# Performance work log

Hardware: AMD Instinct MI355X
Metric: run time of the kernel (lower is better)

The kernel has to match this reference:

```python
import jax, jax.numpy as jnp
import numpy as np

H = 256            # hidden_dim
E = H // 2         # uniform_dim = 128
NH = 4             # num_heads
DH = E // NH       # head_dim = 32
OUT = 256          # output_dim
B = 65536
LN_EPS = 1e-5


def _lin(k, din, dout):
    kw, kb = jax.random.split(k)
    bound = 1.0 / np.sqrt(din)
    W = jax.random.uniform(kw, (din, dout), jnp.float32, -bound, bound)
    b = jax.random.uniform(kb, (dout,), jnp.float32, -bound, bound)
    return W, b


def setup_inputs() -> dict:
    key = jax.random.key(0)
    ks = jax.random.split(key, 20)
    x = jax.random.normal(ks[0], (B, 29), jnp.float32)
    # component encoders (Linear + ReLU)
    Wv, bv = _lin(ks[1], 3, H // 4)
    Wm, bm = _lin(ks[2], 5, H // 4)
    Wi, bi = _lin(ks[3], 2, H // 8)
    Wb, bb = _lin(ks[4], 3, H // 8)
    Wc, bc = _lin(ks[5], 6, H // 4)
    Wf, bf = _lin(ks[6], 10, H // 2)
    # projections to uniform_dim
    Pv, pv = _lin(ks[7], H // 4, E)
    Pm, pm = _lin(ks[8], H // 4, E)
    Pi, pi = _lin(ks[9], H // 8, E)
    Pb, pb = _lin(ks[10], H // 8, E)
    Pc, pc = _lin(ks[11], H // 4, E)
    Pf, pf = _lin(ks[12], H // 2, E)
    # multi-head attention (packed QKV in_proj + out_proj), stored as [in,out]
    Wqkv, bqkv = _lin(ks[13], E, 3 * E)
    Wo, bo = _lin(ks[14], E, E)
    # layernorm
    g = jnp.ones((E,), jnp.float32)
    beta = jnp.zeros((E,), jnp.float32)
    # pool projection
    Wp, bp = _lin(ks[15], E, OUT)
    return dict(x=x, Wv=Wv, bv=bv, Wm=Wm, bm=bm, Wi=Wi, bi=bi, Wb=Wb, bb=bb,
                Wc=Wc, bc=bc, Wf=Wf, bf=bf, Pv=Pv, pv=pv, Pm=Pm, pm=pm,
                Pi=Pi, pi=pi, Pb=Pb, pb=pb, Pc=Pc, pc=pc, Pf=Pf, pf=pf,
                Wqkv=Wqkv, bqkv=bqkv, Wo=Wo, bo=bo, g=g, beta=beta, Wp=Wp, bp=bp)


def _forward(x, Wv, bv, Wm, bm, Wi, bi, Wb, bb, Wc, bc, Wf, bf,
             Pv, pv, Pm, pm, Pi, pi, Pb, pb, Pc, pc, Pf, pf,
             Wqkv, bqkv, Wo, bo, g, beta, Wp, bp):
    enc = lambda v, W, b: jax.nn.relu(v @ W + b)
    # component encoders + projections -> 6 tokens of dim E
    t_v = enc(x[:, 0:3], Wv, bv) @ Pv + pv
    t_m = enc(x[:, 3:8], Wm, bm) @ Pm + pm
    t_i = enc(x[:, 8:10], Wi, bi) @ Pi + pi
    t_b = enc(x[:, 10:13], Wb, bb) @ Pb + pb
    t_c = enc(x[:, 13:19], Wc, bc) @ Pc + pc
    t_f = enc(x[:, 19:29], Wf, bf) @ Pf + pf
    tokens = jnp.stack([t_v, t_m, t_i, t_b, t_c, t_f], axis=1)  # [B,6,E]
    Bn = tokens.shape[0]
    # self-attention (torch MultiheadAttention, batch_first, eval mode)
    qkv = tokens @ Wqkv + bqkv                                   # [B,6,3E]
    q, k, v = jnp.split(qkv, 3, axis=-1)
    q = q.reshape(Bn, 6, NH, DH)
    k = k.reshape(Bn, 6, NH, DH)
    v = v.reshape(Bn, 6, NH, DH)
    scores = jnp.einsum('bqhd,bkhd->bhqk', q, k) / np.sqrt(DH)  # [B,H,6,6]
    attn = jax.nn.softmax(scores, axis=-1)
    ctx = jnp.einsum('bhqk,bkhd->bqhd', attn, v).reshape(Bn, 6, E)
    attn_out = ctx @ Wo + bo
    # residual + layernorm
    h = tokens + attn_out
    mu = jnp.mean(h, axis=-1, keepdims=True)
    var = jnp.mean(jnp.square(h - mu), axis=-1, keepdims=True)
    h = (h - mu) * jax.lax.rsqrt(var + LN_EPS) * g + beta
    # mean-pool over 6 tokens, project, relu
    pooled = jnp.mean(h, axis=1)                                 # [B,E]
    return jax.nn.relu(pooled @ Wp + bp)                         # [B,OUT]


def reference(x, Wv, bv, Wm, bm, Wi, bi, Wb, bb, Wc, bc, Wf, bf,
              Pv, pv, Pm, pm, Pi, pi, Pb, pb, Pc, pc, Pf, pf,
              Wqkv, bqkv, Wo, bo, g, beta, Wp, bp):
    return _forward(x, Wv, bv, Wm, bm, Wi, bi, Wb, bb, Wc, bc, Wf, bf,
                    Pv, pv, Pm, pm, Pi, pi, Pb, pb, Pc, pc, Pf, pf,
                    Wqkv, bqkv, Wo, bo, g, beta, Wp, bp)
```

## Files before the change

### kernel.cpp

```cpp
#include <hip/hip_runtime.h>
#include <math.h>

typedef float f32x4 __attribute__((ext_vector_type(4)));
typedef short short8 __attribute__((ext_vector_type(8)));
typedef unsigned short u16;

#define LN_EPS 1e-5f

__device__ __forceinline__ u16 f2bf(float f) {
    unsigned int x = __float_as_uint(f);
    return (u16)((x + 0x7fffu + ((x >> 16) & 1u)) >> 16);
}
__device__ __forceinline__ float bf2f(u16 u) {
    return __uint_as_float(((unsigned int)u) << 16);
}

#define OFF_QKV 0
#define OFF_WO  49152
#define OFF_WP  65536
#define OFF_PV  98304
#define OFF_PM  106496
#define OFF_PI  114688
#define OFF_PB  118784
#define OFF_PC  122880
#define OFF_PF  131072
#define WS_ELEMS 147456

__global__ __launch_bounds__(512) void convert_weights(
    const float* __restrict__ Wqkv, const float* __restrict__ Wo, const float* __restrict__ Wp,
    const float* __restrict__ Pv, const float* __restrict__ Pm, const float* __restrict__ Pi,
    const float* __restrict__ Pb, const float* __restrict__ Pc, const float* __restrict__ Pf,
    u16* __restrict__ ws)
{
    int gid = blockIdx.x * 512 + threadIdx.x;
    if (gid >= WS_ELEMS) return;
    const float* src; int N, Ksteps, local;
    if (gid < OFF_WO)      { src = Wqkv; N = 384; Ksteps = 4; local = gid; }
    else if (gid < OFF_WP) { src = Wo;   N = 128; Ksteps = 4; local = gid - OFF_WO; }
    else if (gid < OFF_PV) { src = Wp;   N = 256; Ksteps = 4; local = gid - OFF_WP; }
    else if (gid < OFF_PM) { src = Pv;   N = 128; Ksteps = 2; local = gid - OFF_PV; }
    else if (gid < OFF_PI) { src = Pm;   N = 128; Ksteps = 2; local = gid - OFF_PM; }
    else if (gid < OFF_PB) { src = Pi;   N = 128; Ksteps = 1; local = gid - OFF_PI; }
    else if (gid < OFF_PC) { src = Pb;   N = 128; Ksteps = 1; local = gid - OFF_PB; }
    else if (gid < OFF_PF) { src = Pc;   N = 128; Ksteps = 2; local = gid - OFF_PC; }
    else                   { src = Pf;   N = 128; Ksteps = 4; local = gid - OFF_PF; }
    int j  = local & 7;
    int l  = (local >> 3) & 63;
    int r2 = local >> 9;
    int kk = r2 % Ksteps;
    int nt = r2 / Ksteps;
    int srow = kk * 32 + (l >> 4) * 8 + j;
    int scol = nt * 16 + (l & 15);
    ws[gid] = f2bf(src[srow * N + scol]);
}

__global__ __launch_bounds__(512, 4) void asmlp_mfma(
    const float* __restrict__ x,
    const float* __restrict__ Wv, const float* __restrict__ bv,
    const float* __restrict__ Wm, const float* __restrict__ bm,
    const float* __restrict__ Wi, const float* __restrict__ bi,
    const float* __restrict__ Wb, const float* __restrict__ bb,
    const float* __restrict__ Wc, const float* __restrict__ bc,
    const float* __restrict__ Wf, const float* __restrict__ bf_,
    const float* __restrict__ pv, const float* __restrict__ pm,
    const float* __restrict__ pi_, const float* __restrict__ pb_,
    const float* __restrict__ pc_, const float* __restrict__ pf_,
    const float* __restrict__ bqkv, const float* __restrict__ bo,
    const float* __restrict__ gg, const float* __restrict__ beta,
    const float* __restrict__ bp,
    const u16* __restrict__ ws,
    float* __restrict__ out)
{
    const int blk  = blockIdx.x;
    const int t    = threadIdx.x;
    const int lane = t & 63;
    const int wv   = t >> 6;
    const int col  = lane & 15;
    const int lg   = lane >> 4;

    __shared__ u16 sm[31872];
    u16*   s_tok  = sm;
    u16*   s_qkv  = sm + 6144;
    u16*   s_ctx  = sm + 24576;
    u16*   s_att  = sm + 30720;
    float* s_x    = (float*)(sm + 24576);
    u16*   s_h    = sm + 25088;
    u16*   s_pool = sm + 30720;
    float* s_out  = (float*)(sm + 6144);

    if (t < 232) s_x[t] = x[(size_t)blk * 232 + t];
    __syncthreads();

    for (int i = 0; i < 6; ++i) {
        int u = t + i * 512;
        int row = u / 384;
        int jj = u - row * 384;
        const float* W; const float* bias; int din, xo, j, dout;
        if (jj < 64)       { W = Wv; bias = bv;  din = 3;  xo = 0;  j = jj;       dout = 64; }
        else if (jj < 128) { W = Wm; bias = bm;  din = 5;  xo = 3;  j = jj - 64;  dout = 64; }
        else if (jj < 160) { W = Wi; bias = bi;  din = 2;  xo = 8;  j = jj - 128; dout = 32; }
        else if (jj < 192) { W = Wb; bias = bb;  din = 3;  xo = 10; j = jj - 160; dout = 32; }
        else if (jj < 256) { W = Wc; bias = bc;  din = 6;  xo = 13; j = jj - 192; dout = 64; }
        else               { W = Wf; bias = bf_; din = 10; xo = 19; j = jj - 256; dout = 128; }
        float acc = bias[j];
        for (int i2 = 0; i2 < din; ++i2) acc += s_x[row * 29 + xo + i2] * W[i2 * dout + j];
        acc = fmaxf(acc, 0.f);
        s_h[((row * 48 + ((jj >> 3) ^ row)) << 3) + (jj & 7)] = f2bf(acc);
    }
    __syncthreads();

    for (int q = 0; q < 6; ++q) {
        int unit = wv * 6 + q;
        int c = unit >> 3, n = unit & 7;
        const float* bias; int ks, hg, wso;
        switch (c) {
            case 0:  bias = pv;  ks = 2; hg = 0;  wso = OFF_PV; break;
            case 1:  bias = pm;  ks = 2; hg = 8;  wso = OFF_PM; break;
            case 2:  bias = pi_; ks = 1; hg = 16; wso = OFF_PI; break;
            case 3:  bias = pb_; ks = 1; hg = 20; wso = OFF_PB; break;
            case 4:  bias = pc_; ks = 2; hg = 24; wso = OFF_PC; break;
            default: bias = pf_; ks = 4; hg = 32; wso = OFF_PF; break;
        }
        float bcol = bias[n * 16 + col];
        f32x4 acc = {bcol, bcol, bcol, bcol};
        int arow = col & 7;
        for (int kk = 0; kk < ks; ++kk) {
            int g = hg + kk * 4 + lg;
            short8 a = *(const short8*)&s_h[(arow * 48 + (g ^ arow)) << 3];
            short8 b = *(const short8*)&ws[wso + (((n * ks + kk) * 64 + lane) << 3)];
            acc = __builtin_amdgcn_mfma_f32_16x16x32_bf16(a, b, acc, 0, 0, 0);
        }
        if (lg < 2) {
            #pragma unroll
            for (int r = 0; r < 4; ++r) {
                int row = lg * 4 + r;
                int tok = c * 8 + row;
                int cn  = n * 16 + col;
                s_tok[((tok * 16 + ((cn >> 3) ^ (tok & 15))) << 3) + (cn & 7)] = f2bf(acc[r]);
            }
        }
    }
    __syncthreads();

    {
        short8 Bf[3][4];
        float  bb_[3];
        #pragma unroll
        for (int ni = 0; ni < 3; ++ni) {
            int n = wv * 3 + ni;
            bb_[ni] = bqkv[n * 16 + col];
            #pragma unroll
            for (int kk = 0; kk < 4; ++kk)
                Bf[ni][kk] = *(const short8*)&ws[OFF_QKV + (((n * 4 + kk) * 64 + lane) << 3)];
        }
        for (int mt = 0; mt < 3; ++mt) {
            int arow = mt * 16 + col;
            short8 A[4];
            #pragma unroll
            for (int kk = 0; kk < 4; ++kk) {
                int g = kk * 4 + lg;
                A[kk] = *(const short8*)&s_tok[(arow * 16 + (g ^ (arow & 15))) << 3];
            }
            #pragma unroll
            for (int ni = 0; ni < 3; ++ni) {
                f32x4 acc = {bb_[ni], bb_[ni], bb_[ni], bb_[ni]};
                #pragma unroll
                for (int kk = 0; kk < 4; ++kk)
                    acc = __builtin_amdgcn_mfma_f32_16x16x32_bf16(A[kk], Bf[ni][kk], acc, 0, 0, 0);
                int cn = (wv * 3 + ni) * 16 + col;
                #pragma unroll
                for (int r = 0; r < 4; ++r) {
                    int row = mt * 16 + lg * 4 + r;
                    s_qkv[((row * 48 + ((cn >> 3) ^ (row & 15))) << 3) + (cn & 7)] = f2bf(acc[r]);
                }
            }
        }
    }
    __syncthreads();

    if (t < 192) {
        int row = t / 24;
        int rem = t - row * 24;
        int h   = rem / 6;
        int qi  = rem - h * 6;
        int tq  = qi * 8 + row;
        float qf[32];
        #pragma unroll
        for (int gi = 0; gi < 4; ++gi) {
            int g = h * 4 + gi;
            short8 v = *(const short8*)&s_qkv[(tq * 48 + (g ^ (tq & 15))) << 3];
            #pragma unroll
            for (int j = 0; j < 8; ++j) qf[gi * 8 + j] = bf2f((u16)v[j]);
        }
        float sc[6];
        #pragma unroll
        for (int ki = 0; ki < 6; ++ki) {
            int tk = ki * 8 + row;
            float d = 0.f;
            #pragma unroll
            for (int gi = 0; gi < 4; ++gi) {
                int g = 16 + h * 4 + gi;
                short8 v = *(const short8*)&s_qkv[(tk * 48 + (g ^ (tk & 15))) << 3];
                #pragma unroll
                for (int j = 0; j < 8; ++j) d += qf[gi * 8 + j] * bf2f((u16)v[j]);
            }
            sc[ki] = d * 0.17677669529663687f;
        }
        float mx = sc[0];
        #pragma unroll
        for (int ki = 1; ki < 6; ++ki) mx = fmaxf(mx, sc[ki]);
        float e[6], s = 0.f;
        #pragma unroll
        for (int ki = 0; ki < 6; ++ki) { e[ki] = __expf(sc[ki] - mx); s += e[ki]; }
        float inv = 1.f / s;
        #pragma unroll
        for (int ki = 0; ki < 6; ++ki)
            s_att[((row * 4 + h) * 6 + qi) * 6 + ki] = f2bf(e[ki] * inv);
    }
    __syncthreads();

    for (int u = t; u < 768; u += 512) {
        int m = u >> 4, gch = u & 15;
        int row = m & 7, qi = m >> 3, h = gch >> 2;
        float accs[8] = {0, 0, 0, 0, 0, 0, 0, 0};
        #pragma unroll
        for (int ki = 0; ki < 6; ++ki) {
            float p = bf2f(s_att[((row * 4 + h) * 6 + qi) * 6 + ki]);
            int tv = ki * 8 + row;
            int g  = 32 + gch;
            short8 v = *(const short8*)&s_qkv[(tv * 48 + (g ^ (tv & 15))) << 3];
            #pragma unroll
            for (int j = 0; j < 8; ++j) accs[j] += p * bf2f((u16)v[j]);
        }
        short8 o;
        #pragma unroll
        for (int j = 0; j < 8; ++j) o[j] = (short)f2bf(accs[j]);
        *(short8*)&s_ctx[(m * 16 + (gch ^ (m & 15))) << 3] = o;
    }
    __syncthreads();

    if (wv < 3) {
        int mt = wv;
        int arow = mt * 16 + col;
        short8 A[4];
        #pragma unroll
        for (int kk = 0; kk < 4; ++kk) {
            int g = kk * 4 + lg;
            A[kk] = *(const short8*)&s_ctx[(arow * 16 + (g ^ (arow & 15))) << 3];
        }
        f32x4 acc[8];
        #pragma unroll
        for (int n = 0; n < 8; ++n) {
            float b = bo[n * 16 + col];
            acc[n] = (f32x4){b, b, b, b};
            #pragma unroll
            for (int kk = 0; kk < 4; ++kk) {
                short8 Bf = *(const short8*)&ws[OFF_WO + (((n * 4 + kk) * 64 + lane) << 3)];
                acc[n] = __builtin_amdgcn_mfma_f32_16x16x32_bf16(A[kk], Bf, acc[n], 0, 0, 0);
            }
        }
        #pragma unroll
        for (int n = 0; n < 8; ++n) {
            int cn = n * 16 + col;
            #pragma unroll
            for (int r = 0; r < 4; ++r) {
                int row = mt * 16 + lg * 4 + r;
                acc[n][r] += bf2f(s_tok[((row * 16 + ((cn >> 3) ^ (row & 15))) << 3) + (cn & 7)]);
            }
        }
        float mu_[4], rs_[4];
        #pragma unroll
        for (int r = 0; r < 4; ++r) {
            float s1 = 0.f, s2 = 0.f;
            #pragma unroll
            for (int n = 0; n < 8; ++n) { float v = acc[n][r]; s1 += v; s2 += v * v; }
            #pragma unroll
            for (int off = 1; off <= 8; off <<= 1) {
                s1 += __shfl_xor(s1, off, 64);
                s2 += __shfl_xor(s2, off, 64);
            }
            float mu  = s1 * (1.f / 128.f);
            float var = s2 * (1.f / 128.f) - mu * mu;
            mu_[r] = mu;
            rs_[r] = rsqrtf(var + LN_EPS);
        }
        #pragma unroll
        for (int n = 0; n < 8; ++n) {
            int cn = n * 16 + col;
            float gw = gg[cn], bw = beta[cn];
            #pragma unroll
            for (int r = 0; r < 4; ++r) {
                int row = mt * 16 + lg * 4 + r;
                float val = (acc[n][r] - mu_[r]) * rs_[r] * gw + bw;
                s_tok[((row * 16 + ((cn >> 3) ^ (row & 15))) << 3) + (cn & 7)] = f2bf(val);
            }
        }
    }
    __syncthreads();

    if (t < 128) {
        int row = t >> 4, gch = t & 15;
        float fa[8] = {0, 0, 0, 0, 0, 0, 0, 0};
        #pragma unroll
        for (int c = 0; c < 6; ++c) {
            int tok = c * 8 + row;
            short8 v = *(const short8*)&s_tok[(tok * 16 + (gch ^ (tok & 15))) << 3];
            #pragma unroll
            for (int j = 0; j < 8; ++j) fa[j] += bf2f((u16)v[j]);
        }
        short8 o;
        #pragma unroll
        for (int j = 0; j < 8; ++j) o[j] = (short)f2bf(fa[j] * (1.f / 6.f));
        *(short8*)&s_pool[(row * 16 + (gch ^ row)) << 3] = o;
    }
    __syncthreads();

    {
        int arow = col & 7;
        short8 A[4];
        #pragma unroll
        for (int kk = 0; kk < 4; ++kk) {
            int g = kk * 4 + lg;
            A[kk] = *(const short8*)&s_pool[(arow * 16 + (g ^ arow)) << 3];
        }
        #pragma unroll
        for (int ni = 0; ni < 2; ++ni) {
            int n = wv * 2 + ni;
            float b = bp[n * 16 + col];
            f32x4 acc = {b, b, b, b};
            #pragma unroll
            for (int kk = 0; kk < 4; ++kk) {
                short8 Bf = *(const short8*)&ws[OFF_WP + (((n * 4 + kk) * 64 + lane) << 3)];
                acc = __builtin_amdgcn_mfma_f32_16x16x32_bf16(A[kk], Bf, acc, 0, 0, 0);
            }
            if (lg < 2) {
                #pragma unroll
                for (int r = 0; r < 4; ++r) {
                    int row = lg * 4 + r;
                    s_out[row * 260 + n * 16 + col] = fmaxf(acc[r], 0.f);
                }
            }
        }
    }
    __syncthreads();

    if (t < 256) {
        int row = t >> 5, c8 = (t & 31) * 8;
        f32x4 v0 = *(const f32x4*)&s_out[row * 260 + c8];
        f32x4 v1 = *(const f32x4*)&s_out[row * 260 + c8 + 4];
        float* dst = out + ((size_t)blk * 8 + row) * 256 + c8;
        *(f32x4*)dst = v0;
        *(f32x4*)(dst + 4) = v1;
    }
}

extern "C" void kernel_launch(void* const* d_in, const int* in_sizes, int n_in,
                              void* d_out, int out_size, void* d_ws, size_t ws_size,
                              hipStream_t stream) {
    const float* x    = (const float*)d_in[0];
    const float* Wv   = (const float*)d_in[1];
    const float* bv   = (const float*)d_in[2];
    const float* Wm   = (const float*)d_in[3];
    const float* bm   = (const float*)d_in[4];
    const float* Wi   = (const float*)d_in[5];
    const float* bi   = (const float*)d_in[6];
    const float* Wb   = (const float*)d_in[7];
    const float* bb   = (const float*)d_in[8];
    const float* Wc   = (const float*)d_in[9];
    const float* bc   = (const float*)d_in[10];
    const float* Wf   = (const float*)d_in[11];
    const float* bf_  = (const float*)d_in[12];
    const float* Pv   = (const float*)d_in[13];
    const float* pv   = (const float*)d_in[14];
    const float* Pm   = (const float*)d_in[15];
    const float* pm   = (const float*)d_in[16];
    const float* Pi   = (const float*)d_in[17];
    const float* pii  = (const float*)d_in[18];
    const float* Pb   = (const float*)d_in[19];
    const float* pb   = (const float*)d_in[20];
    const float* Pc   = (const float*)d_in[21];
    const float* pc   = (const float*)d_in[22];
    const float* Pf   = (const float*)d_in[23];
    const float* pf   = (const float*)d_in[24];
    const float* Wqkv = (const float*)d_in[25];
    const float* bqkv = (const float*)d_in[26];
    const float* Wo   = (const float*)d_in[27];
    const float* bo   = (const float*)d_in[28];
    const float* gg   = (const float*)d_in[29];
    const float* beta = (const float*)d_in[30];
    const float* Wp   = (const float*)d_in[31];
    const float* bp   = (const float*)d_in[32];
    float* out = (float*)d_out;
    u16* ws = (u16*)d_ws;

    convert_weights<<<288, 512, 0, stream>>>(Wqkv, Wo, Wp, Pv, Pm, Pi, Pb, Pc, Pf, ws);

    const int Bn = in_sizes[0] / 29;
    asmlp_mfma<<<Bn / 8, 512, 0, stream>>>(
        x, Wv, bv, Wm, bm, Wi, bi, Wb, bb, Wc, bc, Wf, bf_,
        pv, pm, pii, pb, pc, pf,
        bqkv, bo, gg, beta, bp, ws, out);
}
```

Baseline: 338.1 us.

## Move encoder layers and attention score/context computation onto MFMA

The scalar component-encoder loop is replaced by a block-diagonal bf16 MFMA GEMM, with x split into hi/lo bf16 parts to keep precision. The weights and biases for it are pre-packed in the conversion kernel. Attention scores, softmax via lane shuffles, and the probability-times-V product now run as small MFMA tiles over transposed Q/K and V layouts instead of per-thread scalar dot products. The f32-to-bf16 rounding uses the packed hardware convert instruction. This cuts VALU work and the LDS footprint, at the cost of padding waste in the 6x6 attention tiles and more complex indexing.

```diff
diff --git a/kernel.cpp b/kernel.cpp
--- a/kernel.cpp
+++ b/kernel.cpp
@@ -7,12 +7,14 @@
 
 #define LN_EPS 1e-5f
 
-__device__ __forceinline__ u16 f2bf(float f) {
-    unsigned int x = __float_as_uint(f);
-    return (u16)((x + 0x7fffu + ((x >> 16) & 1u)) >> 16);
+__device__ __forceinline__ unsigned cvt_pk_bf16(float lo, float hi) {
+    unsigned r;
+    asm("v_cvt_pk_bf16_f32 %0, %1, %2" : "=v"(r) : "v"(lo), "v"(hi));
+    return r;
 }
+__device__ __forceinline__ u16 f2bf(float f) { return (u16)cvt_pk_bf16(f, f); }
 __device__ __forceinline__ float bf2f(u16 u) {
-    return __uint_as_float(((unsigned int)u) << 16);
+    return __uint_as_float(((unsigned)u) << 16);
 }
 
 #define OFF_QKV 0
@@ -24,44 +26,72 @@
 #define OFF_PB  118784
 #define OFF_PC  122880
 #define OFF_PF  131072
-#define WS_ELEMS 147456
+#define OFF_WENC 147456
+#define OFF_BENC 172032
+#define CW_TOTAL 172416
 
 __global__ __launch_bounds__(512) void convert_weights(
     const float* __restrict__ Wqkv, const float* __restrict__ Wo, const float* __restrict__ Wp,
     const float* __restrict__ Pv, const float* __restrict__ Pm, const float* __restrict__ Pi,
     const float* __restrict__ Pb, const float* __restrict__ Pc, const float* __restrict__ Pf,
+    const float* __restrict__ Wv, const float* __restrict__ Wm, const float* __restrict__ Wi,
+    const float* __restrict__ Wb, const float* __restrict__ Wc, const float* __restrict__ Wf,
+    const float* __restrict__ bv, const float* __restrict__ bm, const float* __restrict__ bi,
+    const float* __restrict__ bb, const float* __restrict__ bc, const float* __restrict__ bf_,
     u16* __restrict__ ws)
 {
     int gid = blockIdx.x * 512 + threadIdx.x;
-    if (gid >= WS_ELEMS) return;
-    const float* src; int N, Ksteps, local;
-    if (gid < OFF_WO)      { src = Wqkv; N = 384; Ksteps = 4; local = gid; }
-    else if (gid < OFF_WP) { src = Wo;   N = 128; Ksteps = 4; local = gid - OFF_WO; }
-    else if (gid < OFF_PV) { src = Wp;   N = 256; Ksteps = 4; local = gid - OFF_WP; }
-    else if (gid < OFF_PM) { src = Pv;   N = 128; Ksteps = 2; local = gid - OFF_PV; }
-    else if (gid < OFF_PI) { src = Pm;   N = 128; Ksteps = 2; local = gid - OFF_PM; }
-    else if (gid < OFF_PB) { src = Pi;   N = 128; Ksteps = 1; local = gid - OFF_PI; }
-    else if (gid < OFF_PC) { src = Pb;   N = 128; Ksteps = 1; local = gid - OFF_PB; }
-    else if (gid < OFF_PF) { src = Pc;   N = 128; Ksteps = 2; local = gid - OFF_PC; }
-    else                   { src = Pf;   N = 128; Ksteps = 4; local = gid - OFF_PF; }
-    int j  = local & 7;
-    int l  = (local >> 3) & 63;
-    int r2 = local >> 9;
-    int kk = r2 % Ksteps;
-    int nt = r2 / Ksteps;
-    int srow = kk * 32 + (l >> 4) * 8 + j;
-    int scol = nt * 16 + (l & 15);
-    ws[gid] = f2bf(src[srow * N + scol]);
+    if (gid < OFF_WENC) {
+        const float* src; int N, Ksteps, local;
+        if (gid < OFF_WO)      { src = Wqkv; N = 384; Ksteps = 4; local = gid; }
+        else if (gid < OFF_WP) { src = Wo;   N = 128; Ksteps = 4; local = gid - OFF_WO; }
+        else if (gid < OFF_PV) { src = Wp;   N = 256; Ksteps = 4; local = gid - OFF_WP; }
+        else if (gid < OFF_PM) { src = Pv;   N = 128; Ksteps = 2; local = gid - OFF_PV; }
+        else if (gid < OFF_PI) { src = Pm;   N = 128; Ksteps = 2; local = gid - OFF_PM; }
+        else if (gid < OFF_PB) { src = Pi;   N = 128; Ksteps = 1; local = gid - OFF_PI; }
+        else if (gid < OFF_PC) { src = Pb;   N = 128; Ksteps = 1; local = gid - OFF_PB; }
+        else if (gid < OFF_PF) { src = Pc;   N = 128; Ksteps = 2; local = gid - OFF_PC; }
+        else                   { src = Pf;   N = 128; Ksteps = 4; local = gid - OFF_PF; }
+        int j  = local & 7;
+        int l  = (local >> 3) & 63;
+        int r2 = local >> 9;
+        int kk = r2 % Ksteps;
+        int nt = r2 / Ksteps;
+        int srow = kk * 32 + (l >> 4) * 8 + j;
+        int scol = nt * 16 + (l & 15);
+        ws[gid] = f2bf(src[srow * N + scol]);
+    } else if (gid < OFF_BENC) {
+        int local = gid - OFF_WENC;
+        int j = local & 7, l = (local >> 3) & 63, r2 = local >> 9;
+        int kk = r2 & 1, nt = r2 >> 1;
+        int k = kk * 32 + (l >> 4) * 8 + j;
+        int r = k & 31;
+        int scol = nt * 16 + (l & 15);
+        const float* W; int cb, xo, din, dout;
+        if (scol < 64)       { W = Wv; cb = 0;   xo = 0;  din = 3;  dout = 64; }
+        else if (scol < 128) { W = Wm; cb = 64;  xo = 3;  din = 5;  dout = 64; }
+        else if (scol < 160) { W = Wi; cb = 128; xo = 8;  din = 2;  dout = 32; }
+        else if (scol < 192) { W = Wb; cb = 160; xo = 10; din = 3;  dout = 32; }
+        else if (scol < 256) { W = Wc; cb = 192; xo = 13; din = 6;  dout = 64; }
+        else                 { W = Wf; cb = 256; xo = 19; din = 10; dout = 128; }
+        int rr = r - xo;
+        float val = (r < 29 && rr >= 0 && rr < din) ? W[rr * dout + (scol - cb)] : 0.f;
+        ws[gid] = f2bf(val);
+    } else if (gid < CW_TOTAL) {
+        int j = gid - OFF_BENC;
+        const float* b; int off;
+        if (j < 64)       { b = bv;  off = 0; }
+        else if (j < 128) { b = bm;  off = 64; }
+        else if (j < 160) { b = bi;  off = 128; }
+        else if (j < 192) { b = bb;  off = 160; }
+        else if (j < 256) { b = bc;  off = 192; }
+        else              { b = bf_; off = 256; }
+        ((float*)(ws + OFF_BENC))[j] = b[j - off];
+    }
 }
 
 __global__ __launch_bounds__(512, 4) void asmlp_mfma(
     const float* __restrict__ x,
-    const float* __restrict__ Wv, const float* __restrict__ bv,
-    const float* __restrict__ Wm, const float* __restrict__ bm,
-    const float* __restrict__ Wi, const float* __restrict__ bi,
-    const float* __restrict__ Wb, const float* __restrict__ bb,
-    const float* __restrict__ Wc, const float* __restrict__ bc,
-    const float* __restrict__ Wf, const float* __restrict__ bf_,
     const float* __restrict__ pv, const float* __restrict__ pm,
     const float* __restrict__ pi_, const float* __restrict__ pb_,
     const float* __restrict__ pc_, const float* __restrict__ pf_,
@@ -78,37 +108,60 @@
     const int col  = lane & 15;
     const int lg   = lane >> 4;
 
-    __shared__ u16 sm[31872];
+    __shared__ __attribute__((aligned(16))) u16 sm[30720];
     u16*   s_tok  = sm;
-    u16*   s_qkv  = sm + 6144;
-    u16*   s_ctx  = sm + 24576;
-    u16*   s_att  = sm + 30720;
-    float* s_x    = (float*)(sm + 24576);
-    u16*   s_h    = sm + 25088;
-    u16*   s_pool = sm + 30720;
-    float* s_out  = (float*)(sm + 6144);
-
-    if (t < 232) s_x[t] = x[(size_t)blk * 232 + t];
-    __syncthreads();
-
-    for (int i = 0; i < 6; ++i) {
-        int u = t + i * 512;
-        int row = u / 384;
-        int jj = u - row * 384;
-        const float* W; const float* bias; int din, xo, j, dout;
-        if (jj < 64)       { W = Wv; bias = bv;  din = 3;  xo = 0;  j = jj;       dout = 64; }
-        else if (jj < 128) { W = Wm; bias = bm;  din = 5;  xo = 3;  j = jj - 64;  dout = 64; }
-        else if (jj < 160) { W = Wi; bias = bi;  din = 2;  xo = 8;  j = jj - 128; dout = 32; }
-        else if (jj < 192) { W = Wb; bias = bb;  din = 3;  xo = 10; j = jj - 160; dout = 32; }
-        else if (jj < 256) { W = Wc; bias = bc;  din = 6;  xo = 13; j = jj - 192; dout = 64; }
-        else               { W = Wf; bias = bf_; din = 10; xo = 19; j = jj - 256; dout = 128; }
-        float acc = bias[j];
-        for (int i2 = 0; i2 < din; ++i2) acc += s_x[row * 29 + xo + i2] * W[i2 * dout + j];
-        acc = fmaxf(acc, 0.f);
-        s_h[((row * 48 + ((jj >> 3) ^ row)) << 3) + (jj & 7)] = f2bf(acc);
-    }
-    __syncthreads();
-
+    u16*   s_qk   = sm + 6144;
+    u16*   s_vt   = sm + 18432;
+    u16*   s_ppad = sm + 26624;
+    u16*   s_xa   = sm + 18432;
+    u16*   s_h    = sm + 18944;
+    u16*   s_ctx  = sm + 6144;
+    float* s_out  = (float*)(sm + 12288);
+    u16*   s_pool = sm + 26624;
+
+    if (t < 232) {
+        int row = t / 29, cc = t - row * 29;
+        float f = x[(size_t)blk * 232 + t];
+        u16 hi = f2bf(f);
+        float lo = f - bf2f(hi);
+        s_xa[row * 64 + cc]      = hi;
+        s_xa[row * 64 + 32 + cc] = f2bf(lo);
+    }
+    if (t < 48) {
+        int row = t / 6, sl = t - (t / 6) * 6;
+        int k = (sl < 3) ? (29 + sl) : (58 + sl);
+        s_xa[row * 64 + k] = 0;
+    }
+    __syncthreads();
+
+    {
+        int arow = col & 7;
+        short8 A0 = *(const short8*)&s_xa[arow * 64 + lg * 8];
+        short8 A1 = *(const short8*)&s_xa[arow * 64 + 32 + lg * 8];
+        const float* benc = (const float*)(ws + OFF_BENC);
+        #pragma unroll
+        for (int q = 0; q < 3; ++q) {
+            int nt = wv * 3 + q;
+            float b = benc[nt * 16 + col];
+            f32x4 acc = {b, b, b, b};
+            short8 B0 = *(const short8*)&ws[OFF_WENC + (((nt * 2 + 0) * 64 + lane) << 3)];
+            short8 B1 = *(const short8*)&ws[OFF_WENC + (((nt * 2 + 1) * 64 + lane) << 3)];
+            acc = __builtin_amdgcn_mfma_f32_16x16x32_bf16(A0, B0, acc, 0, 0, 0);
+            acc = __builtin_amdgcn_mfma_f32_16x16x32_bf16(A1, B1, acc, 0, 0, 0);
+            if (lg < 2) {
+                #pragma unroll
+                for (int r = 0; r < 4; ++r) {
+                    int row = lg * 4 + r;
+                    int cn = nt * 16 + col;
+                    s_h[((row * 48 + ((cn >> 3) ^ row)) << 3) + (cn & 7)] =
+                        f2bf(fmaxf(acc[r], 0.f));
+                }
+            }
+        }
+    }
+    __syncthreads();
+
+    #pragma unroll
     for (int q = 0; q < 6; ++q) {
         int unit = wv * 6 + q;
         int c = unit >> 3, n = unit & 7;
@@ -153,9 +206,10 @@
             for (int kk = 0; kk < 4; ++kk)
                 Bf[ni][kk] = *(const short8*)&ws[OFF_QKV + (((n * 4 + kk) * 64 + lane) << 3)];
         }
+        { uint2 z; z.x = 0u; z.y = 0u; *(uint2*)&s_vt[t * 16 + 12] = z; }
         for (int mt = 0; mt < 3; ++mt) {
+            short8 A[4];
             int arow = mt * 16 + col;
-            short8 A[4];
             #pragma unroll
             for (int kk = 0; kk < 4; ++kk) {
                 int g = kk * 4 + lg;
@@ -167,75 +221,113 @@
                 #pragma unroll
                 for (int kk = 0; kk < 4; ++kk)
                     acc = __builtin_amdgcn_mfma_f32_16x16x32_bf16(A[kk], Bf[ni][kk], acc, 0, 0, 0);
-                int cn = (wv * 3 + ni) * 16 + col;
+                int cn = wv * 3 + ni;
+                int cg = cn * 16 + col;
+                if (cn < 16) {
+                    int q4 = ((cg >> 3) & 3) << 2;
+                    int tb = (mt * 16 + lg * 4) ^ q4;
+                    uint2 w;
+                    w.x = cvt_pk_bf16(acc[0], acc[1]);
+                    w.y = cvt_pk_bf16(acc[2], acc[3]);
+                    *(uint2*)&s_qk[cg * 48 + tb] = w;
+                } else {
+                    int d = cg - 256;
+                    int h = d >> 5, ch = (d >> 4) & 1, nn = d & 15;
+                    #pragma unroll
+                    for (int r = 0; r < 4; ++r) {
+                        int token = mt * 16 + lg * 4 + r;
+                        int c2 = token >> 3, rb = token & 7;
+                        int g2 = rb * 2 + (h >> 1);
+                        int kidx = (h & 1) * 6 + c2;
+                        s_vt[((g2 * 2 + ch) * 16 + nn) * 16 + kidx] = f2bf(acc[r]);
+                    }
+                }
+            }
+        }
+    }
+    __syncthreads();
+
+    {
+        const int rb = wv;
+        #pragma unroll
+        for (int i = 0; i < 2; ++i) {
+            const int hp = i;
+            int p  = (col >= 6 && col < 12) ? 1 : 0;
+            int qi = (col < 6) ? col : ((col < 12) ? col - 6 : 0);
+            int tt = qi * 8 + rb;
+            int h  = hp * 2 + p;
+            int tsw = tt ^ (lg << 2);
+            int abase = (h * 32 + lg * 8) * 48 + tsw;
+            int bbase = (128 + h * 32 + lg * 8) * 48 + tsw;
+            short8 Aq, Bk;
+            #pragma unroll
+            for (int j = 0; j < 8; ++j) {
+                Aq[j] = (short)s_qk[abase + j * 48];
+                Bk[j] = (short)s_qk[bbase + j * 48];
+            }
+            f32x4 sc = {0.f, 0.f, 0.f, 0.f};
+            sc = __builtin_amdgcn_mfma_f32_16x16x32_bf16(Aq, Bk, sc, 0, 0, 0);
+            u16* pp = s_ppad + (wv * 2 + i) * 256;
+            f32x4 pr4;
+            #pragma unroll
+            for (int r = 0; r < 4; ++r) {
+                int mr = lg * 4 + r;
+                int prr = (mr >= 6 && mr < 12) ? 1 : 0;
+                float v = sc[r] * 0.17677669529663687f;
+                bool inR = (col >= 6 * prr) && (col < 6 * prr + 6);
+                float mv = inR ? v : -1e30f;
+                #pragma unroll
+                for (int off = 1; off < 16; off <<= 1)
+                    mv = fmaxf(mv, __shfl_xor(mv, off, 16));
+                float e = inR ? __expf(v - mv) : 0.f;
+                float s = e;
+                #pragma unroll
+                for (int off = 1; off < 16; off <<= 1)
+                    s += __shfl_xor(s, off, 16);
+                pr4[r] = (mr < 12) ? (e / s) : 0.f;
+            }
+            uint2 w;
+            w.x = cvt_pk_bf16(pr4[0], pr4[1]);
+            w.y = cvt_pk_bf16(pr4[2], pr4[3]);
+            *(uint2*)&pp[col * 16 + lg * 4] = w;
+        }
+    }
+    __syncthreads();
+
+    {
+        const int rb = wv;
+        #pragma unroll
+        for (int i = 0; i < 2; ++i) {
+            const int hp = i;
+            u16* pp = s_ppad + (wv * 2 + i) * 256;
+            short8 Ap;
+            if (lg < 2) {
+                #pragma unroll
+                for (int j = 0; j < 8; ++j)
+                    Ap[j] = (short)pp[(lg * 8 + j) * 16 + col];
+            } else {
+                #pragma unroll
+                for (int j = 0; j < 8; ++j) Ap[j] = 0;
+            }
+            int g2 = rb * 2 + hp;
+            #pragma unroll
+            for (int ch = 0; ch < 2; ++ch) {
+                short8 Bv = *(const short8*)&s_vt[(((g2 * 2 + ch) * 16 + col) * 16) + ((lg & 1) * 8)];
+                f32x4 c = {0.f, 0.f, 0.f, 0.f};
+                c = __builtin_amdgcn_mfma_f32_16x16x32_bf16(Ap, Bv, c, 0, 0, 0);
                 #pragma unroll
                 for (int r = 0; r < 4; ++r) {
-                    int row = mt * 16 + lg * 4 + r;
-                    s_qkv[((row * 48 + ((cn >> 3) ^ (row & 15))) << 3) + (cn & 7)] = f2bf(acc[r]);
+                    int mr = lg * 4 + r;
+                    if (mr < 12) {
+                        int pq = mr >= 6 ? 1 : 0;
+                        int qi = mr - 6 * pq;
+                        int token = qi * 8 + rb;
+                        int d = (hp * 2 + pq) * 32 + ch * 16 + col;
+                        s_ctx[((token * 16 + ((d >> 3) ^ (token & 15))) << 3) + (d & 7)] = f2bf(c[r]);
+                    }
                 }
             }
         }
-    }
-    __syncthreads();
-
-    if (t < 192) {
-        int row = t / 24;
-        int rem = t - row * 24;
-        int h   = rem / 6;
-        int qi  = rem - h * 6;
-        int tq  = qi * 8 + row;
-        float qf[32];
-        #pragma unroll
-        for (int gi = 0; gi < 4; ++gi) {
-            int g = h * 4 + gi;
-            short8 v = *(const short8*)&s_qkv[(tq * 48 + (g ^ (tq & 15))) << 3];
-            #pragma unroll
-            for (int j = 0; j < 8; ++j) qf[gi * 8 + j] = bf2f((u16)v[j]);
-        }
-        float sc[6];
-        #pragma unroll
-        for (int ki = 0; ki < 6; ++ki) {
-            int tk = ki * 8 + row;
-            float d = 0.f;
-            #pragma unroll
-            for (int gi = 0; gi < 4; ++gi) {
-                int g = 16 + h * 4 + gi;
-                short8 v = *(const short8*)&s_qkv[(tk * 48 + (g ^ (tk & 15))) << 3];
-                #pragma unroll
-                for (int j = 0; j < 8; ++j) d += qf[gi * 8 + j] * bf2f((u16)v[j]);
-            }
-            sc[ki] = d * 0.17677669529663687f;
-        }
-        float mx = sc[0];
-        #pragma unroll
-        for (int ki = 1; ki < 6; ++ki) mx = fmaxf(mx, sc[ki]);
-        float e[6], s = 0.f;
-        #pragma unroll
-        for (int ki = 0; ki < 6; ++ki) { e[ki] = __expf(sc[ki] - mx); s += e[ki]; }
-        float inv = 1.f / s;
-        #pragma unroll
-        for (int ki = 0; ki < 6; ++ki)
-            s_att[((row * 4 + h) * 6 + qi) * 6 + ki] = f2bf(e[ki] * inv);
-    }
-    __syncthreads();
-
-    for (int u = t; u < 768; u += 512) {
-        int m = u >> 4, gch = u & 15;
-        int row = m & 7, qi = m >> 3, h = gch >> 2;
-        float accs[8] = {0, 0, 0, 0, 0, 0, 0, 0};
-        #pragma unroll
-        for (int ki = 0; ki < 6; ++ki) {
-            float p = bf2f(s_att[((row * 4 + h) * 6 + qi) * 6 + ki]);
-            int tv = ki * 8 + row;
-            int g  = 32 + gch;
-            short8 v = *(const short8*)&s_qkv[(tv * 48 + (g ^ (tv & 15))) << 3];
-            #pragma unroll
-            for (int j = 0; j < 8; ++j) accs[j] += p * bf2f((u16)v[j]);
-        }
-        short8 o;
-        #pragma unroll
-        for (int j = 0; j < 8; ++j) o[j] = (short)f2bf(accs[j]);
-        *(short8*)&s_ctx[(m * 16 + (gch ^ (m & 15))) << 3] = o;
     }
     __syncthreads();
 
@@ -393,11 +485,12 @@
     float* out = (float*)d_out;
     u16* ws = (u16*)d_ws;
 
-    convert_weights<<<288, 512, 0, stream>>>(Wqkv, Wo, Wp, Pv, Pm, Pi, Pb, Pc, Pf, ws);
+    convert_weights<<<(CW_TOTAL + 511) / 512, 512, 0, stream>>>(
+        Wqkv, Wo, Wp, Pv, Pm, Pi, Pb, Pc, Pf,
+        Wv, Wm, Wi, Wb, Wc, Wf, bv, bm, bi, bb, bc, bf_, ws);
 
     const int Bn = in_sizes[0] / 29;
     asmlp_mfma<<<Bn / 8, 512, 0, stream>>>(
-        x, Wv, bv, Wm, bm, Wi, bi, Wb, bb, Wc, bc, Wf, bf_,
-        pv, pm, pii, pb, pc, pf,
+        x, pv, pm, pii, pb, pc, pf,
         bqkv, bo, gg, beta, bp, ws, out);
 }
```

Result: faster. 309.8 us (-8.4%).
